# Optimization experiments

Hardware: AMD Instinct MI355X
Metric: run time of the kernel (lower is better)

## Reference

```python
import jax, jax.numpy as jnp
import numpy as np

B, N = 8, 2048
HYPER, IN_F, OUT_F = 128, 64, 64
ALPHA = 0.2  # LeakyReLU negative slope
NEG_INF = -9e15


def setup_inputs() -> dict:
    key = jax.random.key(0)
    k1, k2, k3, k4, k5, k6 = jax.random.split(key, 6)
    state = jax.random.normal(k1, (B, HYPER), dtype=jnp.float32)
    h = jax.random.normal(k2, (B, N, IN_F), dtype=jnp.float32)
    adj = jax.random.randint(k3, (B, N, N), 0, 2, dtype=jnp.int32)
    # hypernetwork linear: weight [in*out, hyper] (torch layout), bias [in*out]
    lim = 1.0 / np.sqrt(HYPER)
    Wp_w = jax.random.uniform(k4, (IN_F * OUT_F, HYPER), minval=-lim, maxval=lim, dtype=jnp.float32)
    Wp_b = jax.random.uniform(k5, (IN_F * OUT_F,), minval=-lim, maxval=lim, dtype=jnp.float32)
    # attention vector a [2*out, 1], xavier_uniform gain=1.414
    ga = 1.414 * np.sqrt(6.0 / (2 * OUT_F + 1))
    a = jax.random.uniform(k6, (2 * OUT_F, 1), minval=-ga, maxval=ga, dtype=jnp.float32)
    return {"state": state, "h": h, "adj": adj, "Wp_w": Wp_w, "Wp_b": Wp_b, "a": a}


def reference(state, h, adj, Wp_w, Wp_b, a):
    # hypernetwork-generated weight: abs(Linear(state)) -> [B, in, out]
    W = jnp.abs(state @ Wp_w.T + Wp_b).reshape(-1, IN_F, OUT_F)
    Wh = jnp.einsum('bni,bio->bno', h, W)          # [B, N, out]
    Wh1 = Wh @ a[:OUT_F, :]                        # [B, N, 1]
    Wh2 = Wh @ a[OUT_F:, :]                        # [B, N, 1]
    e = jax.nn.leaky_relu(Wh1 + jnp.transpose(Wh2, (0, 2, 1)), negative_slope=ALPHA)  # [B, N, N]
    scores = jnp.where(adj > 0, e, NEG_INF)
    attention = jax.nn.softmax(scores, axis=1)     # softmax over dim=1 as in original
    h_prime = jnp.einsum('bmn,bmo->bno', jnp.transpose(attention, (0, 2, 1)), Wh) if False else attention @ Wh
    return jax.nn.elu(h_prime)                     # concat=True
```

## Files before the change

kernel.cpp:

```cpp
#include <hip/hip_runtime.h>
#include <hip/hip_bf16.h>
#include <hip/hip_fp16.h>

#define B_ 8
#define N_ 2048
#define ALPHA_ 0.2f
#define LOG2E_ 1.44269504088896f

#define OFF_WB    0u
#define OFF_WA1   65536u
#define OFF_WA2   67584u
#define OFF_WH1   69632u
#define OFF_WH2   135168u
#define OFF_DEN   200704u
#define OFF_WHBT  266240u
#define OFF_MASK  2363392u

typedef _Float16 half8_t __attribute__((ext_vector_type(8)));
typedef float f32x4_t __attribute__((ext_vector_type(4)));
union UH { unsigned u[4]; half8_t s; };

__device__ __forceinline__ unsigned pkh(float a, float b) {
  __half2 h = __floats2half2_rn(a, b);
  return *(unsigned*)&h;
}
__device__ __forceinline__ unsigned pk2(float lo, float hi) {
  return ((__float_as_uint(hi) + 0x8000u) & 0xFFFF0000u) |
         ((__float_as_uint(lo) + 0x8000u) >> 16);
}

__global__ __launch_bounds__(256) void k1_hyperw(
    const float* __restrict__ state, const float* __restrict__ Wpw,
    const float* __restrict__ Wpb, const float* __restrict__ av,
    unsigned short* __restrict__ Wb, float* __restrict__ Wa1,
    float* __restrict__ Wa2) {
  int b = blockIdx.y;
  int r = blockIdx.x * 256 + threadIdx.x;
  int lane = threadIdx.x & 63;
  int i = r >> 6, o = r & 63;
  __shared__ float st[128];
  if (threadIdx.x < 128) st[threadIdx.x] = state[b * 128 + threadIdx.x];
  __syncthreads();
  float acc = Wpb[r];
  const float4* wp = (const float4*)(Wpw + (size_t)r * 128);
  #pragma unroll 8
  for (int hh = 0; hh < 32; ++hh) {
    float4 v = wp[hh];
    acc += st[hh*4]*v.x + st[hh*4+1]*v.y + st[hh*4+2]*v.z + st[hh*4+3]*v.w;
  }
  float wv = fabsf(acc);
  __half hw = __float2half(wv);
  Wb[b * 4096 + o * 64 + i] = *(unsigned short*)&hw;
  float p1 = wv * av[lane];
  float p2 = wv * av[64 + lane];
  #pragma unroll
  for (int off = 32; off > 0; off >>= 1) {
    p1 += __shfl_xor(p1, off);
    p2 += __shfl_xor(p2, off);
  }
  if (lane == 0) { Wa1[b * 64 + i] = p1; Wa2[b * 64 + i] = p2; }
}

__global__ __launch_bounds__(256) void k2_wh(
    const float* __restrict__ h, const unsigned short* __restrict__ Wb,
    const float* __restrict__ Wa1, const float* __restrict__ Wa2,
    float* __restrict__ Wh1, float* __restrict__ Wh2,
    unsigned short* __restrict__ WhbT) {
  int b = blockIdx.y;
  int tid = threadIdx.x, lane = tid & 63;
  int w = tid >> 6;
  int n0 = blockIdx.x * 64 + w * 16;
  int l15 = lane & 15, kg = lane >> 4;
  int row = n0 + l15;
  const float* hrow = h + (((size_t)b * N_ + row) << 6);
  float4 ha0 = *(const float4*)(hrow + kg * 8);
  float4 ha1 = *(const float4*)(hrow + kg * 8 + 4);
  float4 hb0 = *(const float4*)(hrow + 32 + kg * 8);
  float4 hb1 = *(const float4*)(hrow + 32 + kg * 8 + 4);
  const float* wa1 = Wa1 + b * 64;
  const float* wa2 = Wa2 + b * 64;
  float4 A0 = *(const float4*)(wa1 + kg * 8),      A1 = *(const float4*)(wa1 + kg * 8 + 4);
  float4 A2 = *(const float4*)(wa1 + 32 + kg * 8), A3 = *(const float4*)(wa1 + 32 + kg * 8 + 4);
  float4 C0 = *(const float4*)(wa2 + kg * 8),      C1 = *(const float4*)(wa2 + kg * 8 + 4);
  float4 C2 = *(const float4*)(wa2 + 32 + kg * 8), C3 = *(const float4*)(wa2 + 32 + kg * 8 + 4);
  float v1 = ha0.x*A0.x + ha0.y*A0.y + ha0.z*A0.z + ha0.w*A0.w
           + ha1.x*A1.x + ha1.y*A1.y + ha1.z*A1.z + ha1.w*A1.w
           + hb0.x*A2.x + hb0.y*A2.y + hb0.z*A2.z + hb0.w*A2.w
           + hb1.x*A3.x + hb1.y*A3.y + hb1.z*A3.z + hb1.w*A3.w;
  float v2 = ha0.x*C0.x + ha0.y*C0.y + ha0.z*C0.z + ha0.w*C0.w
           + ha1.x*C1.x + ha1.y*C1.y + ha1.z*C1.z + ha1.w*C1.w
           + hb0.x*C2.x + hb0.y*C2.y + hb0.z*C2.z + hb0.w*C2.w
           + hb1.x*C3.x + hb1.y*C3.y + hb1.z*C3.z + hb1.w*C3.w;
  v1 += __shfl_xor(v1, 16); v1 += __shfl_xor(v1, 32);
  v2 += __shfl_xor(v2, 16); v2 += __shfl_xor(v2, 32);
  if (lane < 16) {
    Wh1[b * N_ + row] = v1 * LOG2E_;
    Wh2[b * N_ + row] = v2 * LOG2E_;
  }
  UH ua, ub;
  ua.u[0] = pkh(ha0.x, ha0.y); ua.u[1] = pkh(ha0.z, ha0.w);
  ua.u[2] = pkh(ha1.x, ha1.y); ua.u[3] = pkh(ha1.z, ha1.w);
  ub.u[0] = pkh(hb0.x, hb0.y); ub.u[1] = pkh(hb0.z, hb0.w);
  ub.u[2] = pkh(hb1.x, hb1.y); ub.u[3] = pkh(hb1.z, hb1.w);
  const unsigned short* wbb = Wb + b * 4096;
  f32x4_t acc[4];
  #pragma unroll
  for (int of = 0; of < 4; ++of) acc[of] = {0.f, 0.f, 0.f, 0.f};
  #pragma unroll
  for (int of = 0; of < 4; ++of) {
    int o = of * 16 + l15;
    half8_t b0 = *(const half8_t*)(wbb + o * 64 + kg * 8);
    half8_t b1 = *(const half8_t*)(wbb + o * 64 + 32 + kg * 8);
    acc[of] = __builtin_amdgcn_mfma_f32_16x16x32_f16(ua.s, b0, acc[of], 0, 0, 0);
    acc[of] = __builtin_amdgcn_mfma_f32_16x16x32_f16(ub.s, b1, acc[of], 0, 0, 0);
  }
  int nb = n0 + (kg << 2);
  #pragma unroll
  for (int of = 0; of < 4; ++of) {
    int o = of * 16 + l15;
    uint2 pk;
    pk.x = pkh(acc[of][0], acc[of][1]);
    pk.y = pkh(acc[of][2], acc[of][3]);
    *(uint2*)(WhbT + ((size_t)(b * 64 + o)) * N_ + nb) = pk;
  }
}

#define K3_PROC(VV, UVV, II)                                                 \
  do {                                                                       \
    bool p0 = (VV).x > 0, p1 = (VV).y > 0, p2 = (VV).z > 0, p3 = (VV).w > 0; \
    unsigned long long b0 = __ballot(p0), b1 = __ballot(p1);                 \
    unsigned long long b2 = __ballot(p2), b3 = __ballot(p3);                 \
    unsigned long long bsel = qsel == 0 ? b0 : qsel == 1 ? b1                \
                            : qsel == 2 ? b2 : b3;                           \
    wreg = (rsel == (II)) ? bsel : wreg;                                     \
    den0 += p0 ? fmaxf((UVV).x, (UVV).y * b2c0) : 0.f;                       \
    den1 += p1 ? fmaxf((UVV).x, (UVV).y * b2c1) : 0.f;                       \
    den2 += p2 ? fmaxf((UVV).x, (UVV).y * b2c2) : 0.f;                       \
    den3 += p3 ? fmaxf((UVV).x, (UVV).y * b2c3) : 0.f;                       \
  } while (0)

__global__ __launch_bounds__(256) void k3_mask(
    const int* __restrict__ adj, const float* __restrict__ Wh1,
    const float* __restrict__ Wh2, float* __restrict__ den,
    unsigned long long* __restrict__ maskQ) {
  int jg = blockIdx.x, ic = blockIdx.y, b = blockIdx.z;
  int tid = threadIdx.x, lane = tid & 63, w = tid >> 6;
  int i0 = ic * 64 + w * 16;
  __shared__ float2 uvs[64];
  __shared__ float red[4][256];
  if (tid < 64) {
    float w1v = Wh1[b * N_ + ic * 64 + tid];
    uvs[tid] = make_float2(exp2f(w1v), exp2f(0.2f * w1v));
  }
  __syncthreads();
  float2 uv0 = uvs[(w<<4)+0],  uv1 = uvs[(w<<4)+1],  uv2 = uvs[(w<<4)+2],  uv3 = uvs[(w<<4)+3];
  float2 uv4 = uvs[(w<<4)+4],  uv5 = uvs[(w<<4)+5],  uv6 = uvs[(w<<4)+6],  uv7 = uvs[(w<<4)+7];
  float2 uv8 = uvs[(w<<4)+8],  uv9 = uvs[(w<<4)+9],  uvA = uvs[(w<<4)+10], uvB = uvs[(w<<4)+11];
  float2 uvC = uvs[(w<<4)+12], uvD = uvs[(w<<4)+13], uvE = uvs[(w<<4)+14], uvF = uvs[(w<<4)+15];
  int j0 = jg * 256 + 4 * lane;
  float4 wh2v = *(const float4*)(Wh2 + b * N_ + j0);
  float b2c0 = exp2f(-0.8f * wh2v.x), b2c1 = exp2f(-0.8f * wh2v.y);
  float b2c2 = exp2f(-0.8f * wh2v.z), b2c3 = exp2f(-0.8f * wh2v.w);
  const int4* ap = (const int4*)(adj + ((size_t)(b * N_ + i0)) * N_ + jg * 256);
  const size_t rs = N_ / 4;
  int qsel = lane & 3, rsel = lane >> 2;
  unsigned long long wreg = 0;
  float den0 = 0.f, den1 = 0.f, den2 = 0.f, den3 = 0.f;
  int4 r0 = ap[0 * rs + lane], r1 = ap[1 * rs + lane];
  int4 r2 = ap[2 * rs + lane], r3 = ap[3 * rs + lane];
  int4 r4 = ap[4 * rs + lane], r5 = ap[5 * rs + lane];
  int4 r6 = ap[6 * rs + lane], r7 = ap[7 * rs + lane];
  K3_PROC(r0, uv0, 0);  r0 = ap[8 * rs + lane];
  K3_PROC(r1, uv1, 1);  r1 = ap[9 * rs + lane];
  K3_PROC(r2, uv2, 2);  r2 = ap[10 * rs + lane];
  K3_PROC(r3, uv3, 3);  r3 = ap[11 * rs + lane];
  K3_PROC(r4, uv4, 4);  r4 = ap[12 * rs + lane];
  K3_PROC(r5, uv5, 5);  r5 = ap[13 * rs + lane];
  K3_PROC(r6, uv6, 6);  r6 = ap[14 * rs + lane];
  K3_PROC(r7, uv7, 7);  r7 = ap[15 * rs + lane];
  K3_PROC(r0, uv8, 8);  K3_PROC(r1, uv9, 9);  K3_PROC(r2, uvA, 10); K3_PROC(r3, uvB, 11);
  K3_PROC(r4, uvC, 12); K3_PROC(r5, uvD, 13); K3_PROC(r6, uvE, 14); K3_PROC(r7, uvF, 15);
  maskQ[((((size_t)b * 8 + jg) * 2048 + i0 + rsel) << 2) + qsel] = wreg;
  red[w][(lane << 2) + 0] = den0;
  red[w][(lane << 2) + 1] = den1;
  red[w][(lane << 2) + 2] = den2;
  red[w][(lane << 2) + 3] = den3;
  __syncthreads();
  float dsum = red[0][tid] + red[1][tid] + red[2][tid] + red[3][tid];
  atomicAdd(den + b * N_ + jg * 256 + tid, dsum);
}

__global__ __launch_bounds__(256) void k4_mfma(
    const unsigned long long* __restrict__ maskQ, const float* __restrict__ Wh1,
    const float* __restrict__ Wh2, const float* __restrict__ den,
    const unsigned short* __restrict__ WhbT, float* __restrict__ out) {
  int ib = blockIdx.x, b = blockIdx.y;
  int tid = threadIdx.x, lane = tid & 63;
  int w = __builtin_amdgcn_readfirstlane(tid >> 6);
  int is = w & 1, kh = w >> 1;
  extern __shared__ __align__(16) unsigned char smem[];
  unsigned* abL = (unsigned*)(smem + 32768);
  const unsigned short* wsrc = WhbT + (size_t)b * 64 * N_;
  int oo = tid >> 4, s5 = tid & 15;
  int swz = (s5 * 16) ^ ((oo & 7) << 4);
  uint4 sv0, sv1, sv2, sv3, sv4, sv5, sv6, sv7;
#define SLOAD(RR)                                                              \
  { const unsigned short* s_ = wsrc + (size_t)oo * N_ + (RR) * 128 + s5 * 8;   \
    sv0 = *(const uint4*)(s_);                                                 \
    sv1 = *(const uint4*)(s_ + 16 * N_);                                       \
    sv2 = *(const uint4*)(s_ + 32 * N_);                                       \
    sv3 = *(const uint4*)(s_ + 48 * N_);                                       \
    sv4 = *(const uint4*)(s_ + 1024);                                          \
    sv5 = *(const uint4*)(s_ + 16 * N_ + 1024);                                \
    sv6 = *(const uint4*)(s_ + 32 * N_ + 1024);                                \
    sv7 = *(const uint4*)(s_ + 48 * N_ + 1024); }
#define SWRITE()                                                               \
  { unsigned char* d_ = smem + oo * 256 + swz;                                 \
    *(uint4*)(d_)                 = sv0;                                       \
    *(uint4*)(d_ + 16 * 256)      = sv1;                                       \
    *(uint4*)(d_ + 32 * 256)      = sv2;                                       \
    *(uint4*)(d_ + 48 * 256)      = sv3;                                       \
    *(uint4*)(d_ + 16384)         = sv4;                                       \
    *(uint4*)(d_ + 16384 + 16*256)= sv5;                                       \
    *(uint4*)(d_ + 16384 + 32*256)= sv6;                                       \
    *(uint4*)(d_ + 16384 + 48*256)= sv7; }
  SLOAD(0)
  #pragma unroll
  for (int q = 0; q < 8; ++q) {
    int j = (q << 8) + tid;
    float dv = den[b * N_ + j];
    float inv = 1.0f / fmaxf(dv, 1e-37f);
    float B4 = exp2f(-0.8f * Wh2[b * N_ + j]) * inv;
    abL[j] = pk2(B4, inv);
  }
  SWRITE()
  int l15 = lane & 15, lg = lane >> 4;
  int i0 = (ib << 5) + (is << 4);
  int i = i0 + l15;
  float w1 = Wh1[b * N_ + i];
  float u = exp2f(w1), v = exp2f(0.2f * w1);
  f32x4_t acc[4];
  #pragma unroll
  for (int of = 0; of < 4; ++of) acc[of] = {0.f, 0.f, 0.f, 0.f};
  unsigned char* mybt = smem + kh * 16384;
  const unsigned long long* mbase = maskQ + (size_t)b * 8 * 2048 * 4;
  for (int rr = 0; rr < 8; ++rr) {
    __syncthreads();
    if (rr < 7) SLOAD(rr + 1)
    int tg = kh * 8 + rr;
    int jg = tg >> 1, r2 = tg & 1;
    const uint4* qp = (const uint4*)(mbase + (((size_t)jg * 2048 + i) << 2));
    uint4 q0 = qp[0], q1 = qp[1];
    unsigned long long Wq[4];
    Wq[0] = ((unsigned long long)q0.y << 32) | q0.x;
    Wq[1] = ((unsigned long long)q0.w << 32) | q0.z;
    Wq[2] = ((unsigned long long)q1.y << 32) | q1.x;
    Wq[3] = ((unsigned long long)q1.w << 32) | q1.z;
    #pragma unroll
    for (int jt2 = 0; jt2 < 2; ++jt2) {
      #pragma unroll
      for (int s = 0; s < 2; ++s) {
        int jfull = kh * 1024 + rr * 128 + jt2 * 64 + s * 32 + lg * 8;
        int tbase = r2 * 32 + jt2 * 16 + s * 8 + lg * 2;
        unsigned m[4];
        #pragma unroll
        for (int k2 = 0; k2 < 4; ++k2)
          m[k2] = (unsigned)(Wq[k2] >> tbase) & 3u;
        const uint4* abp = (const uint4*)&abL[jfull];
        uint4 a0 = abp[0], a1 = abp[1];
        unsigned aw[8] = {a0.x, a0.y, a0.z, a0.w, a1.x, a1.y, a1.z, a1.w};
        UH A;
        #pragma unroll
        for (int p2 = 0; p2 < 4; ++p2) {
          int e0 = 2 * p2, e1 = 2 * p2 + 1;
          float A40 = __uint_as_float(aw[e0] & 0xFFFF0000u);
          float B40 = __uint_as_float(aw[e0] << 16);
          float A41 = __uint_as_float(aw[e1] & 0xFFFF0000u);
          float B41 = __uint_as_float(aw[e1] << 16);
          float plo = fmaxf(u * A40, v * B40);
          float phi = fmaxf(u * A41, v * B41);
          plo = (m[e0 & 3] & (1u << (e0 >> 2))) ? plo : 0.f;
          phi = (m[e1 & 3] & (1u << (e1 >> 2))) ? phi : 0.f;
          A.u[p2] = pkh(plo, phi);
        }
        int boff = jt2 * 128 + s * 64 + lg * 16;
        #pragma unroll
        for (int of = 0; of < 4; ++of) {
          int o = (of << 4) + l15;
          half8_t bv = *(const half8_t*)(mybt + o * 256 + (boff ^ ((o & 7) << 4)));
          acc[of] = __builtin_amdgcn_mfma_f32_16x16x32_f16(A.s, bv, acc[of], 0, 0, 0);
        }
      }
    }
    __syncthreads();
    if (rr < 7) SWRITE()
  }
  __syncthreads();
  float* fred = (float*)smem;
  if (kh == 1) {
    #pragma unroll
    for (int of = 0; of < 4; ++of)
      *(f32x4_t*)(fred + (((is << 6) + lane) << 4) + (of << 2)) = acc[of];
  }
  __syncthreads();
  if (kh == 0) {
    #pragma unroll
    for (int of = 0; of < 4; ++of) {
      f32x4_t oth = *(const f32x4_t*)(fred + (((is << 6) + lane) << 4) + (of << 2));
      #pragma unroll
      for (int q = 0; q < 4; ++q) {
        float xv = acc[of][q] + oth[q];
        xv = xv > 0.f ? xv : (__expf(xv) - 1.f);
        out[((size_t)(b * N_ + i0 + (lg << 2) + q)) * 64 + (of << 4) + l15] = xv;
      }
    }
  }
}

extern "C" void kernel_launch(void* const* d_in, const int* in_sizes, int n_in,
                              void* d_out, int out_size, void* d_ws, size_t ws_size,
                              hipStream_t stream) {
  const float* state = (const float*)d_in[0];
  const float* h     = (const float*)d_in[1];
  const int*   adj   = (const int*)d_in[2];
  const float* Wpw   = (const float*)d_in[3];
  const float* Wpb   = (const float*)d_in[4];
  const float* av    = (const float*)d_in[5];
  float* out = (float*)d_out;
  char* ws = (char*)d_ws;
  unsigned short* Wb = (unsigned short*)(ws + OFF_WB);
  float* Wa1  = (float*)(ws + OFF_WA1);
  float* Wa2  = (float*)(ws + OFF_WA2);
  float* Wh1  = (float*)(ws + OFF_WH1);
  float* Wh2  = (float*)(ws + OFF_WH2);
  float* den  = (float*)(ws + OFF_DEN);
  unsigned short* WhbT = (unsigned short*)(ws + OFF_WHBT);
  unsigned long long* maskQ = (unsigned long long*)(ws + OFF_MASK);

  hipMemsetAsync(den, 0, B_ * N_ * sizeof(float), stream);
  hipLaunchKernelGGL(k1_hyperw, dim3(16, 8), dim3(256), 0, stream,
                     state, Wpw, Wpb, av, Wb, Wa1, Wa2);
  hipLaunchKernelGGL(k2_wh, dim3(32, 8), dim3(256), 0, stream,
                     h, Wb, Wa1, Wa2, Wh1, Wh2, WhbT);
  hipLaunchKernelGGL(k3_mask, dim3(8, 32, 8), dim3(256), 0, stream,
                     adj, Wh1, Wh2, den, maskQ);
  hipLaunchKernelGGL(k4_mfma, dim3(64, 8), dim3(256), 40960, stream,
                     maskQ, Wh1, Wh2, den, WhbT, out);
}
```

Before: 63.44 us.

## Split softmax denominator out of mask kernel into separate bitmask-driven kernel

The mask-packing kernel now only reads adj and writes the ballot bitmask. A new kernel computes the column softmax denominators from the packed bitmask held in LDS, with fewer atomics per element. This makes the adj-streaming kernel lighter and purely bandwidth-bound, at the cost of an extra launch and a rereading of the mask.

```diff
diff --git a/kernel.cpp b/kernel.cpp
--- a/kernel.cpp
+++ b/kernel.cpp
@@ -125,69 +125,71 @@
   }
 }
 
-#define K3_PROC(VV, UVV, II)                                                 \
+#define K3M(VV, II)                                                          \
   do {                                                                       \
-    bool p0 = (VV).x > 0, p1 = (VV).y > 0, p2 = (VV).z > 0, p3 = (VV).w > 0; \
-    unsigned long long b0 = __ballot(p0), b1 = __ballot(p1);                 \
-    unsigned long long b2 = __ballot(p2), b3 = __ballot(p3);                 \
-    unsigned long long bsel = qsel == 0 ? b0 : qsel == 1 ? b1                \
+    unsigned long long b0 = __ballot((VV).x > 0), b1 = __ballot((VV).y > 0); \
+    unsigned long long b2 = __ballot((VV).z > 0), b3 = __ballot((VV).w > 0); \
+    unsigned long long bsel = qsel == 0 ? b0 : qsel == 1 ? b1               \
                             : qsel == 2 ? b2 : b3;                           \
     wreg = (rsel == (II)) ? bsel : wreg;                                     \
-    den0 += p0 ? fmaxf((UVV).x, (UVV).y * b2c0) : 0.f;                       \
-    den1 += p1 ? fmaxf((UVV).x, (UVV).y * b2c1) : 0.f;                       \
-    den2 += p2 ? fmaxf((UVV).x, (UVV).y * b2c2) : 0.f;                       \
-    den3 += p3 ? fmaxf((UVV).x, (UVV).y * b2c3) : 0.f;                       \
   } while (0)
 
 __global__ __launch_bounds__(256) void k3_mask(
-    const int* __restrict__ adj, const float* __restrict__ Wh1,
-    const float* __restrict__ Wh2, float* __restrict__ den,
-    unsigned long long* __restrict__ maskQ) {
+    const int* __restrict__ adj, unsigned long long* __restrict__ maskQ) {
   int jg = blockIdx.x, ic = blockIdx.y, b = blockIdx.z;
   int tid = threadIdx.x, lane = tid & 63, w = tid >> 6;
   int i0 = ic * 64 + w * 16;
-  __shared__ float2 uvs[64];
-  __shared__ float red[4][256];
-  if (tid < 64) {
-    float w1v = Wh1[b * N_ + ic * 64 + tid];
-    uvs[tid] = make_float2(exp2f(w1v), exp2f(0.2f * w1v));
-  }
-  __syncthreads();
-  float2 uv0 = uvs[(w<<4)+0],  uv1 = uvs[(w<<4)+1],  uv2 = uvs[(w<<4)+2],  uv3 = uvs[(w<<4)+3];
-  float2 uv4 = uvs[(w<<4)+4],  uv5 = uvs[(w<<4)+5],  uv6 = uvs[(w<<4)+6],  uv7 = uvs[(w<<4)+7];
-  float2 uv8 = uvs[(w<<4)+8],  uv9 = uvs[(w<<4)+9],  uvA = uvs[(w<<4)+10], uvB = uvs[(w<<4)+11];
-  float2 uvC = uvs[(w<<4)+12], uvD = uvs[(w<<4)+13], uvE = uvs[(w<<4)+14], uvF = uvs[(w<<4)+15];
-  int j0 = jg * 256 + 4 * lane;
-  float4 wh2v = *(const float4*)(Wh2 + b * N_ + j0);
-  float b2c0 = exp2f(-0.8f * wh2v.x), b2c1 = exp2f(-0.8f * wh2v.y);
-  float b2c2 = exp2f(-0.8f * wh2v.z), b2c3 = exp2f(-0.8f * wh2v.w);
   const int4* ap = (const int4*)(adj + ((size_t)(b * N_ + i0)) * N_ + jg * 256);
   const size_t rs = N_ / 4;
   int qsel = lane & 3, rsel = lane >> 2;
   unsigned long long wreg = 0;
-  float den0 = 0.f, den1 = 0.f, den2 = 0.f, den3 = 0.f;
   int4 r0 = ap[0 * rs + lane], r1 = ap[1 * rs + lane];
   int4 r2 = ap[2 * rs + lane], r3 = ap[3 * rs + lane];
   int4 r4 = ap[4 * rs + lane], r5 = ap[5 * rs + lane];
   int4 r6 = ap[6 * rs + lane], r7 = ap[7 * rs + lane];
-  K3_PROC(r0, uv0, 0);  r0 = ap[8 * rs + lane];
-  K3_PROC(r1, uv1, 1);  r1 = ap[9 * rs + lane];
-  K3_PROC(r2, uv2, 2);  r2 = ap[10 * rs + lane];
-  K3_PROC(r3, uv3, 3);  r3 = ap[11 * rs + lane];
-  K3_PROC(r4, uv4, 4);  r4 = ap[12 * rs + lane];
-  K3_PROC(r5, uv5, 5);  r5 = ap[13 * rs + lane];
-  K3_PROC(r6, uv6, 6);  r6 = ap[14 * rs + lane];
-  K3_PROC(r7, uv7, 7);  r7 = ap[15 * rs + lane];
-  K3_PROC(r0, uv8, 8);  K3_PROC(r1, uv9, 9);  K3_PROC(r2, uvA, 10); K3_PROC(r3, uvB, 11);
-  K3_PROC(r4, uvC, 12); K3_PROC(r5, uvD, 13); K3_PROC(r6, uvE, 14); K3_PROC(r7, uvF, 15);
+  K3M(r0, 0);  r0 = ap[8 * rs + lane];
+  K3M(r1, 1);  r1 = ap[9 * rs + lane];
+  K3M(r2, 2);  r2 = ap[10 * rs + lane];
+  K3M(r3, 3);  r3 = ap[11 * rs + lane];
+  K3M(r4, 4);  r4 = ap[12 * rs + lane];
+  K3M(r5, 5);  r5 = ap[13 * rs + lane];
+  K3M(r6, 6);  r6 = ap[14 * rs + lane];
+  K3M(r7, 7);  r7 = ap[15 * rs + lane];
+  K3M(r0, 8);  K3M(r1, 9);  K3M(r2, 10); K3M(r3, 11);
+  K3M(r4, 12); K3M(r5, 13); K3M(r6, 14); K3M(r7, 15);
   maskQ[((((size_t)b * 8 + jg) * 2048 + i0 + rsel) << 2) + qsel] = wreg;
-  red[w][(lane << 2) + 0] = den0;
-  red[w][(lane << 2) + 1] = den1;
-  red[w][(lane << 2) + 2] = den2;
-  red[w][(lane << 2) + 3] = den3;
+}
+
+__global__ __launch_bounds__(256) void k3d_den(
+    const unsigned long long* __restrict__ maskQ, const float* __restrict__ Wh1,
+    const float* __restrict__ Wh2, float* __restrict__ den) {
+  int jg = blockIdx.x, ic = blockIdx.y, b = blockIdx.z;
+  int tid = threadIdx.x;
+  __shared__ float2 uvs[256];
+  __shared__ unsigned long long wlds[256 * 4];
+  {
+    const uint4* src = (const uint4*)(maskQ + ((((size_t)b * 8 + jg) * 2048 + ic * 256) << 2));
+    uint4* dst = (uint4*)wlds;
+    dst[tid] = src[tid];
+    dst[tid + 256] = src[tid + 256];
+  }
+  {
+    float w1 = Wh1[b * N_ + ic * 256 + tid];
+    uvs[tid] = make_float2(exp2f(w1), exp2f(0.2f * w1));
+  }
+  int j = jg * 256 + tid;
+  float B2 = exp2f(-0.8f * Wh2[b * N_ + j]);
   __syncthreads();
-  float dsum = red[0][tid] + red[1][tid] + red[2][tid] + red[3][tid];
-  atomicAdd(den + b * N_ + jg * 256 + tid, dsum);
+  int q = tid & 3, t = tid >> 2;
+  float d = 0.f;
+  #pragma unroll 8
+  for (int i = 0; i < 256; ++i) {
+    unsigned long long word = wlds[i * 4 + q];
+    float2 uv = uvs[i];
+    float val = fmaxf(uv.x, uv.y * B2);
+    d += ((word >> t) & 1ull) ? val : 0.f;
+  }
+  atomicAdd(den + b * N_ + j, d);
 }
 
 __global__ __launch_bounds__(256) void k4_mfma(
@@ -342,8 +344,9 @@
                      state, Wpw, Wpb, av, Wb, Wa1, Wa2);
   hipLaunchKernelGGL(k2_wh, dim3(32, 8), dim3(256), 0, stream,
                      h, Wb, Wa1, Wa2, Wh1, Wh2, WhbT);
-  hipLaunchKernelGGL(k3_mask, dim3(8, 32, 8), dim3(256), 0, stream,
-                     adj, Wh1, Wh2, den, maskQ);
+  hipLaunchKernelGGL(k3_mask, dim3(8, 32, 8), dim3(256), 0, stream, adj, maskQ);
+  hipLaunchKernelGGL(k3d_den, dim3(8, 8, 8), dim3(256), 0, stream,
+                     maskQ, Wh1, Wh2, den);
   hipLaunchKernelGGL(k4_mfma, dim3(64, 8), dim3(256), 40960, stream,
                      maskQ, Wh1, Wh2, den, WhbT, out);
 }
```

After: 69.92 us. +10.2%, slower.
